# Optimization experiments

Hardware: AMD Instinct MI355X
Metric: run time of the kernel (lower is better)

The kernel has to match this reference:

```python
import math
import jax, jax.numpy as jnp
import numpy as np

DIM = 192
HEADS = 4
OUT_DIM = 192

def _conv(x, w, groups=1, pad=0):
    return jax.lax.conv_general_dilated(
        x, w, window_strides=(1, 1), padding=[(pad, pad), (pad, pad)],
        feature_group_count=groups, dimension_numbers=('NCHW', 'OIHW', 'NCHW'))

def setup_inputs() -> dict:
    key = jax.random.key(0)
    ks = jax.random.split(key, 8)
    b, c, h, w = 8, DIM, 128, 128
    x = jax.random.normal(ks[0], (b, c, h, w), dtype=jnp.float32)
    y = jax.random.normal(ks[1], (b, c, h, w), dtype=jnp.float32)
    s = 0.02
    kv_w = jax.random.normal(ks[2], (2 * DIM, DIM, 1, 1), dtype=jnp.float32) * s
    kv_dw_w = jax.random.normal(ks[3], (2 * DIM, 1, 3, 3), dtype=jnp.float32) * s  # depthwise, groups=2*dim
    q_w = jax.random.normal(ks[4], (DIM, DIM, 1, 1), dtype=jnp.float32) * s
    q_dw_w = jax.random.normal(ks[5], (DIM, DIM, 3, 3), dtype=jnp.float32) * s  # dense 3x3 (groups=1 in source)
    proj_w = jax.random.normal(ks[6], (OUT_DIM, DIM, 1, 1), dtype=jnp.float32) * s
    temperature = jnp.ones((HEADS, 1, 1), dtype=jnp.float32)
    return {"x": x, "y": y, "kv_w": kv_w, "kv_dw_w": kv_dw_w, "q_w": q_w,
            "q_dw_w": q_dw_w, "proj_w": proj_w, "temperature": temperature}

def _l2norm(t, eps=1e-12):
    # matches torch F.normalize(dim=-1)
    n = jnp.sqrt(jnp.sum(t * t, axis=-1, keepdims=True))
    return t / jnp.maximum(n, eps)

def reference(x, y, kv_w, kv_dw_w, q_w, q_dw_w, proj_w, temperature):
    b, c, h, w = x.shape
    hw = h * w
    ch = c // HEADS  # channels per head
    kv = _conv(_conv(x, kv_w), kv_dw_w, groups=2 * c, pad=1)  # [b, 2c, h, w]
    k, v = jnp.split(kv, 2, axis=1)
    q = _conv(_conv(y, q_w), q_dw_w, pad=1)  # [b, c, h, w]
    # b (head ch) h w -> b head ch (h w)
    q = q.reshape(b, HEADS, ch, hw)
    k = k.reshape(b, HEADS, ch, hw)
    v = v.reshape(b, HEADS, ch, hw)
    q = _l2norm(q)
    k = _l2norm(k)
    attn = jnp.einsum('bhcn,bhdn->bhcd', q, k)  # channel-wise attention [b,H,ch,ch]
    temp = temperature * math.log(attn.shape[-1])  # [H,1,1]
    attn = jax.nn.softmax(attn * temp[None], axis=-1)
    out = jnp.einsum('bhcd,bhdn->bhcn', attn, v)  # [b,H,ch,hw]
    out = out.reshape(b, c, h, w)
    return _conv(out, proj_w)
```

## Files before the change

### kernel.cpp

```cpp
#include <hip/hip_runtime.h>


#define HW 16384

using f32x4  = __attribute__((ext_vector_type(4))) float;
using bf16x8 = __attribute__((ext_vector_type(8))) __bf16;
using u16x8  = __attribute__((ext_vector_type(8))) unsigned short;
typedef unsigned short u16;

__device__ __forceinline__ u16 f2bf(float f) {
  unsigned u = __builtin_bit_cast(unsigned, f);
  u = (u + 0x7fffu + ((u >> 16) & 1u)) >> 16;
  return (u16)u;
}
__device__ __forceinline__ float bf2f(u16 s) {
  unsigned u = ((unsigned)s) << 16;
  return __builtin_bit_cast(float, u);
}

__device__ __forceinline__ void g2l16(const void* g, void* l) {
  __builtin_amdgcn_global_load_lds(
      (const __attribute__((address_space(1))) unsigned int*)g,
      (__attribute__((address_space(3))) unsigned int*)l, 16, 0, 0);
}

__global__ __launch_bounds__(256) void pack_w1(
    const float* __restrict__ kv_w, u16* __restrict__ W1) {
  int i = blockIdx.x * 256 + threadIdx.x;
  W1[i] = f2bf(kv_w[i]);
}

__global__ __launch_bounds__(192) void make_w4(
    const float* __restrict__ q_w, const float* __restrict__ q_dw_w,
    u16* __restrict__ W4) {
  const int o = blockIdx.x / 9, seg = blockIdx.x % 9;
  const int c = threadIdx.x;
  float s = 0.f;
  for (int ic = 0; ic < 192; ++ic)
    s += q_dw_w[(o * 192 + ic) * 9 + seg] * q_w[ic * 192 + c];
  W4[o * 1728 + seg * 192 + c] = f2bf(s);
}

template <typename TIn>
__global__ __launch_bounds__(256) void transpose_kernel(
    const TIn* __restrict__ src, u16* __restrict__ dst, int srcCstride) {
  __shared__ u16 tile[32][34];
  const int bz = blockIdx.z;
  const int n0 = blockIdx.x * 32;
  const int c0 = blockIdx.y * 32;
  const TIn* s = src + (long)bz * srcCstride * HW;
  u16* d = dst + (long)bz * HW * 192;
  const int tx = threadIdx.x & 31;
  const int ty = threadIdx.x >> 5;
#pragma unroll
  for (int i = 0; i < 32; i += 8) {
    if constexpr (sizeof(TIn) == 4)
      tile[ty + i][tx] = f2bf(((const float*)s)[(long)(c0 + ty + i) * HW + n0 + tx]);
    else
      tile[ty + i][tx] = ((const u16*)s)[(long)(c0 + ty + i) * HW + n0 + tx];
  }
  __syncthreads();
#pragma unroll
  for (int i = 0; i < 32; i += 8)
    d[(long)(n0 + ty + i) * 192 + c0 + tx] = tile[tx][ty + i];
}

template <int NSEG, bool OUT_BF16, bool FUSE_RQ>
__global__ __launch_bounds__(256, 2) void gemm_kernel(
    const u16* __restrict__ A, const u16* __restrict__ Bt,
    void* __restrict__ Cout, const u16* __restrict__ zp,
    int M, long aBatchStride, float* __restrict__ rqs) {
  __shared__ __align__(16) u16 shA[2][4096];
  __shared__ __align__(16) u16 shB[2][16384];
  const int Ktot = NSEG * 192;
  const int NT = NSEG * 3;
  const int tid = threadIdx.x;
  const int w = tid >> 6;
  const int lane = tid & 63;
  const int rl = lane & 15;
  const int q4 = lane >> 4;
  const int wm = w & 1, wn = w >> 1;
  const int b = blockIdx.z;
  const int n0 = blockIdx.x * 256;
  const int m0 = blockIdx.y * 64;

  const u16* Ab = A + (long)b * aBatchStride + (long)m0 * Ktot;
  const u16* Btb = Bt + (long)b * HW * 192;
  const char* asrc = (const char*)(Ab + (long)(w * 16 + rl) * Ktot) + q4 * 16;
  const char* zpp = (const char*)zp + q4 * 16;

  const char* p0[4];
  int xx[4], yy[4];
#pragma unroll
  for (int j = 0; j < 4; ++j) {
    int n = n0 + (w * 4 + j) * 16 + rl;
    p0[j] = (const char*)(Btb + (long)n * 192) + q4 * 16;
    xx[j] = n & 127;
    yy[j] = n >> 7;
  }

  f32x4 acc[2][8];
#pragma unroll
  for (int i = 0; i < 2; ++i)
#pragma unroll
    for (int j = 0; j < 8; ++j) acc[i][j] = f32x4{0.f, 0.f, 0.f, 0.f};

  const int lane_off = lane * 8;

  auto stage = [&](int t, int sbuf) {
    const long ao = (long)t * 128;
    g2l16(asrc + ao, &shA[sbuf][w * 1024]);
    g2l16(asrc + ao + 64, &shA[sbuf][w * 1024 + 512]);
    const char* bp[4];
    int kb;
    if constexpr (NSEG == 1) {
      kb = t * 128;
#pragma unroll
      for (int j = 0; j < 4; ++j) bp[j] = p0[j];
    } else {
      const int seg = t / 3;
      kb = (t - seg * 3) * 128;
      const int dy = seg / 3 - 1, dx = seg % 3 - 1;
      const int roff = (dy * 128 + dx) * 384;
#pragma unroll
      for (int j = 0; j < 4; ++j) {
        bool ok = ((unsigned)(xx[j] + dx) < 128u) && ((unsigned)(yy[j] + dy) < 128u);
        bp[j] = ok ? p0[j] + roff : zpp;
      }
    }
#pragma unroll
    for (int j = 0; j < 4; ++j) {
      g2l16(bp[j] + kb, &shB[sbuf][(w * 4 + j) * 1024]);
      g2l16(bp[j] + kb + 64, &shB[sbuf][(w * 4 + j) * 1024 + 512]);
    }
  };

  auto compute = [&](int cbuf) {
    bf16x8 af[2][2];
#pragma unroll
    for (int i = 0; i < 2; ++i)
#pragma unroll
      for (int h = 0; h < 2; ++h)
        af[i][h] = *(const bf16x8*)&shA[cbuf][(wm * 2 + i) * 1024 + h * 512 + lane_off];
#pragma unroll
    for (int jh = 0; jh < 2; ++jh) {
      bf16x8 bfr[4][2];
#pragma unroll
      for (int j2 = 0; j2 < 4; ++j2)
#pragma unroll
        for (int h = 0; h < 2; ++h)
          bfr[j2][h] = *(const bf16x8*)&shB[cbuf][(wn * 8 + jh * 4 + j2) * 1024 + h * 512 + lane_off];
#pragma unroll
      for (int i = 0; i < 2; ++i)
#pragma unroll
        for (int j2 = 0; j2 < 4; ++j2) {
          const int j = jh * 4 + j2;
          acc[i][j] = __builtin_amdgcn_mfma_f32_16x16x32_bf16(af[i][0], bfr[j2][0], acc[i][j], 0, 0, 0);
          acc[i][j] = __builtin_amdgcn_mfma_f32_16x16x32_bf16(af[i][1], bfr[j2][1], acc[i][j], 0, 0, 0);
        }
    }
  };

  stage(0, 0);
  __syncthreads();
  int cur = 0;
  for (int t = 0; t < NT - 1; ++t) {
    stage(t + 1, cur ^ 1);
    compute(cur);
    __syncthreads();
    cur ^= 1;
  }
  compute(cur);

  const int mb = m0 + wm * 32;
  const int nb = n0 + wn * 128;
  if constexpr (OUT_BF16) {
    u16* Cb = (u16*)Cout + (long)b * M * HW;
#pragma unroll
    for (int i = 0; i < 2; ++i)
#pragma unroll
      for (int j = 0; j < 8; ++j)
#pragma unroll
        for (int r = 0; r < 4; ++r)
          Cb[(long)(mb + i * 16 + q4 * 4 + r) * HW + nb + j * 16 + rl] = f2bf(acc[i][j][r]);
  } else {
    float* Cb = (float*)Cout + (long)b * M * HW;
#pragma unroll
    for (int i = 0; i < 2; ++i)
#pragma unroll
      for (int j = 0; j < 8; ++j)
#pragma unroll
        for (int r = 0; r < 4; ++r)
          Cb[(long)(mb + i * 16 + q4 * 4 + r) * HW + nb + j * 16 + rl] = acc[i][j][r];
  }
  if constexpr (FUSE_RQ) {
#pragma unroll
    for (int i = 0; i < 2; ++i)
#pragma unroll
      for (int r = 0; r < 4; ++r) {
        float s = 0.f;
#pragma unroll
        for (int j = 0; j < 8; ++j) s += acc[i][j][r] * acc[i][j][r];
        s += __shfl_xor(s, 1, 64);
        s += __shfl_xor(s, 2, 64);
        s += __shfl_xor(s, 4, 64);
        s += __shfl_xor(s, 8, 64);
        if (rl == 0)
          atomicAdd(&rqs[b * 192 + mb + i * 16 + q4 * 4 + r], s);
      }
  }
}

template <bool FUSE_NORM>
__global__ __launch_bounds__(256) void dwconv_kernel(
    const u16* __restrict__ kv, const float* __restrict__ dww,
    u16* __restrict__ dst, int cbase, int dstCstride, float* __restrict__ rks) {
  __shared__ __align__(16) u16 sp[HW];
  const int c = blockIdx.x;
  const int b = blockIdx.y;
  const int c2 = cbase + c;
  const u16* src = kv + ((long)b * 384 + c2) * HW;
  u16* out = dst + ((long)b * dstCstride + c) * HW;
  const int tid = threadIdx.x;
#pragma unroll
  for (int it = 0; it < 8; ++it)
    ((u16x8*)sp)[it * 256 + tid] = ((const u16x8*)src)[it * 256 + tid];
  __syncthreads();
  float w9[9];
#pragma unroll
  for (int t = 0; t < 9; ++t) w9[t] = dww[c2 * 9 + t];
  float ssum = 0.f;
  for (int o = 0; o < 8; ++o) {
    const int base = o * 2048 + tid * 8;
    const int yy = base >> 7;
    const int x0 = base & 127;
    float vv[3][10];
#pragma unroll
    for (int r = 0; r < 3; ++r) {
      int yr = yy + r - 1;
      if (yr >= 0 && yr < 128) {
        const u16* rp = sp + yr * 128 + x0;
        u16x8 mid = *(const u16x8*)rp;
#pragma unroll
        for (int i2 = 0; i2 < 8; ++i2) vv[r][1 + i2] = bf2f(mid[i2]);
        vv[r][0] = (x0 > 0)   ? bf2f(rp[-1]) : 0.f;
        vv[r][9] = (x0 < 120) ? bf2f(rp[8])  : 0.f;
      } else {
#pragma unroll
        for (int i2 = 0; i2 < 10; ++i2) vv[r][i2] = 0.f;
      }
    }
    u16x8 ov;
#pragma unroll
    for (int i2 = 0; i2 < 8; ++i2) {
      float s = 0.f;
#pragma unroll
      for (int r = 0; r < 3; ++r)
#pragma unroll
        for (int d = 0; d < 3; ++d) s += w9[r * 3 + d] * vv[r][i2 + d];
      if constexpr (FUSE_NORM) ssum += s * s;
      ov[i2] = f2bf(s);
    }
    *(u16x8*)(out + base) = ov;
  }
  if constexpr (FUSE_NORM) {
#pragma unroll
    for (int off = 32; off; off >>= 1) ssum += __shfl_down(ssum, off, 64);
    if ((tid & 63) == 0) atomicAdd(&rks[b * 192 + c], ssum);
  }
}

__global__ __launch_bounds__(256) void gram_kernel(
    const u16* __restrict__ qq, const u16* __restrict__ kk, float* __restrict__ gram) {
  __shared__ float red[4 * 2304];
  const int bh = blockIdx.x;
  const int kc = blockIdx.y;
  const int b = bh >> 2, h = bh & 3;
  const u16* qb = qq + ((long)b * 192 + h * 48) * HW;
  const u16* kb = kk + ((long)b * 192 + h * 48) * HW;
  const int tid = threadIdx.x, w = tid >> 6, lane = tid & 63;
  const int rl = lane & 15, q4 = lane >> 4;
  f32x4 acc[3][3];
#pragma unroll
  for (int i = 0; i < 3; ++i)
#pragma unroll
    for (int j = 0; j < 3; ++j) acc[i][j] = f32x4{0.f, 0.f, 0.f, 0.f};
  for (int tt = 0; tt < 16; ++tt) {
    const int k0 = ((kc * 16 + tt) * 4 + w) * 32 + q4 * 8;
    bf16x8 af[3], bfr[3];
#pragma unroll
    for (int i = 0; i < 3; ++i) af[i] = *(const bf16x8*)(qb + (long)(i * 16 + rl) * HW + k0);
#pragma unroll
    for (int j = 0; j < 3; ++j) bfr[j] = *(const bf16x8*)(kb + (long)(j * 16 + rl) * HW + k0);
#pragma unroll
    for (int i = 0; i < 3; ++i)
#pragma unroll
      for (int j = 0; j < 3; ++j)
        acc[i][j] = __builtin_amdgcn_mfma_f32_16x16x32_bf16(af[i], bfr[j], acc[i][j], 0, 0, 0);
  }
#pragma unroll
  for (int i = 0; i < 3; ++i)
#pragma unroll
    for (int j = 0; j < 3; ++j)
#pragma unroll
      for (int r = 0; r < 4; ++r)
        red[w * 2304 + (i * 16 + q4 * 4 + r) * 48 + j * 16 + rl] = acc[i][j][r];
  __syncthreads();
  for (int e = tid; e < 2304; e += 256)
    atomicAdd(&gram[(long)bh * 2304 + e], red[e] + red[2304 + e] + red[4608 + e] + red[6912 + e]);
}

__global__ __launch_bounds__(64) void softmax_kernel(
    const float* __restrict__ gram, const float* __restrict__ rqs,
    const float* __restrict__ rks, const float* __restrict__ temperature,
    float* __restrict__ attn) {
  const int R = blockIdx.x;
  const int lane = threadIdx.x;
  const int b = R / 192;
  const int h = (R % 192) / 48;
  const float ts = temperature[h] * 3.8712010109078907f;
  const float rq = rsqrtf(fmaxf(rqs[R], 1e-24f));
  float val = -3.0e38f;
  if (lane < 48) {
    const float rk = rsqrtf(fmaxf(rks[b * 192 + h * 48 + lane], 1e-24f));
    val = gram[(long)R * 48 + lane] * rq * rk * ts;
  }
  float mx = val;
#pragma unroll
  for (int off = 32; off; off >>= 1) mx = fmaxf(mx, __shfl_xor(mx, off, 64));
  float ex = (lane < 48) ? expf(val - mx) : 0.f;
  float sm = ex;
#pragma unroll
  for (int off = 32; off; off >>= 1) sm += __shfl_xor(sm, off, 64);
  if (lane < 48) attn[(long)R * 48 + lane] = ex / sm;
}

__global__ __launch_bounds__(192) void pa_kernel(
    const float* __restrict__ proj_w, const float* __restrict__ attn,
    u16* __restrict__ PA) {
  const int b = blockIdx.x;
  const int o = blockIdx.y;
  const int dg = threadIdx.x;
  const int hg = dg / 48, dl = dg % 48;
  const float* arow = attn + ((long)(b * 4 + hg) * 48) * 48 + dl;
  const float* prow = proj_w + o * 192 + hg * 48;
  float s = 0.f;
#pragma unroll
  for (int cl = 0; cl < 48; ++cl) s += prow[cl] * arow[(long)cl * 48];
  PA[((long)b * 192 + o) * 192 + dg] = f2bf(s);
}

extern "C" void kernel_launch(void* const* d_in, const int* in_sizes, int n_in,
                              void* d_out, int out_size, void* d_ws, size_t ws_size,
                              hipStream_t stream) {
  (void)in_sizes; (void)n_in; (void)out_size; (void)ws_size;
  const float* x        = (const float*)d_in[0];
  const float* y        = (const float*)d_in[1];
  const float* kv_w     = (const float*)d_in[2];
  const float* kv_dw_w  = (const float*)d_in[3];
  const float* q_w      = (const float*)d_in[4];
  const float* q_dw_w   = (const float*)d_in[5];
  const float* proj_w   = (const float*)d_in[6];
  const float* temperature = (const float*)d_in[7];

  char* ws = (char*)d_ws;
  u16* KV = (u16*)(ws + 0L);
  u16* R0 = (u16*)(ws + 100663296L);
  u16* R1 = (u16*)(ws + 150994944L);
  u16* R2 = (u16*)(ws + 201326592L);
  char* tail = ws + 251658240L;
  u16*   zp   = (u16*)(tail + 0);
  float* rqs  = (float*)(tail + 512);
  float* rks  = (float*)(tail + 6656);
  float* gram = (float*)(tail + 12800);
  float* attn = (float*)(tail + 307712);
  u16*   W1   = (u16*)(tail + 602624);
  u16*   W4   = (u16*)(tail + 750080);
  u16*   PA   = (u16*)(tail + 1413632);

  hipMemsetAsync(tail, 0, 307712, stream);
  pack_w1<<<288, 256, 0, stream>>>(kv_w, W1);
  make_w4<<<1728, 192, 0, stream>>>(q_w, q_dw_w, W4);

  transpose_kernel<float><<<dim3(512, 6, 8), 256, 0, stream>>>(y, R2, 192);
  gemm_kernel<9, true, true><<<dim3(64, 3, 8), 256, 0, stream>>>(W4, R2, R1, zp, 192, 0, rqs);

  transpose_kernel<float><<<dim3(512, 6, 8), 256, 0, stream>>>(x, R2, 192);
  gemm_kernel<1, true, false><<<dim3(64, 6, 8), 256, 0, stream>>>(W1, R2, KV, zp, 384, 0, nullptr);
  dwconv_kernel<true><<<dim3(192, 8), 256, 0, stream>>>(KV, kv_dw_w, R0, 0, 192, rks);
  dwconv_kernel<false><<<dim3(192, 8), 256, 0, stream>>>(KV, kv_dw_w, KV, 192, 384, nullptr);
  transpose_kernel<u16><<<dim3(512, 6, 8), 256, 0, stream>>>(KV, R2, 384);

  gram_kernel<<<dim3(32, 8), 256, 0, stream>>>(R1, R0, gram);
  softmax_kernel<<<1536, 64, 0, stream>>>(gram, rqs, rks, temperature, attn);
  pa_kernel<<<dim3(8, 192), 192, 0, stream>>>(proj_w, attn, PA);
  gemm_kernel<1, false, false><<<dim3(64, 3, 8), 256, 0, stream>>>(PA, R2, d_out, zp, 192, 36864, nullptr);
}
```

Baseline: 681.3 us.

## Enlarge GEMM tile to 192x256 with 512 threads and deeper async pipeline

```diff
diff --git a/kernel.cpp b/kernel.cpp
--- a/kernel.cpp
+++ b/kernel.cpp
@@ -66,11 +66,11 @@
 }
 
 template <int NSEG, bool OUT_BF16, bool FUSE_RQ>
-__global__ __launch_bounds__(256, 2) void gemm_kernel(
+__global__ __launch_bounds__(512, 2) void gemm_kernel(
     const u16* __restrict__ A, const u16* __restrict__ Bt,
     void* __restrict__ Cout, const u16* __restrict__ zp,
     int M, long aBatchStride, float* __restrict__ rqs) {
-  __shared__ __align__(16) u16 shA[2][4096];
+  __shared__ __align__(16) u16 shA[2][12288];
   __shared__ __align__(16) u16 shB[2][16384];
   const int Ktot = NSEG * 192;
   const int NT = NSEG * 3;
@@ -79,128 +79,135 @@
   const int lane = tid & 63;
   const int rl = lane & 15;
   const int q4 = lane >> 4;
-  const int wm = w & 1, wn = w >> 1;
+  const int wm = w >> 2, wn = w & 3;
   const int b = blockIdx.z;
   const int n0 = blockIdx.x * 256;
-  const int m0 = blockIdx.y * 64;
+  const int m0 = blockIdx.y * 192;
 
   const u16* Ab = A + (long)b * aBatchStride + (long)m0 * Ktot;
   const u16* Btb = Bt + (long)b * HW * 192;
-  const char* asrc = (const char*)(Ab + (long)(w * 16 + rl) * Ktot) + q4 * 16;
   const char* zpp = (const char*)zp + q4 * 16;
 
-  const char* p0[4];
-  int xx[4], yy[4];
-#pragma unroll
-  for (int j = 0; j < 4; ++j) {
-    int n = n0 + (w * 4 + j) * 16 + rl;
-    p0[j] = (const char*)(Btb + (long)n * 192) + q4 * 16;
-    xx[j] = n & 127;
-    yy[j] = n >> 7;
-  }
-
-  f32x4 acc[2][8];
-#pragma unroll
-  for (int i = 0; i < 2; ++i)
-#pragma unroll
-    for (int j = 0; j < 8; ++j) acc[i][j] = f32x4{0.f, 0.f, 0.f, 0.f};
+  const char* aptr0 = (const char*)(Ab + (long)(w * 16 + rl) * Ktot) + q4 * 16;
+  const char* aptr1 = (const char*)(Ab + (long)((8 + (w >> 1)) * 16 + rl) * Ktot)
+                      + q4 * 16 + (w & 1) * 64;
+
+  const char* p0b[2];
+  int xx[2], yy[2];
+#pragma unroll
+  for (int jj = 0; jj < 2; ++jj) {
+    int n = n0 + (2 * w + jj) * 16 + rl;
+    p0b[jj] = (const char*)(Btb + (long)n * 192) + q4 * 16;
+    xx[jj] = n & 127;
+    yy[jj] = n >> 7;
+  }
+
+  f32x4 acc[6][4];
+#pragma unroll
+  for (int i = 0; i < 6; ++i)
+#pragma unroll
+    for (int j = 0; j < 4; ++j) acc[i][j] = f32x4{0.f, 0.f, 0.f, 0.f};
 
   const int lane_off = lane * 8;
 
-  auto stage = [&](int t, int sbuf) {
-    const long ao = (long)t * 128;
-    g2l16(asrc + ao, &shA[sbuf][w * 1024]);
-    g2l16(asrc + ao + 64, &shA[sbuf][w * 1024 + 512]);
-    const char* bp[4];
-    int kb;
+  auto stage = [&](int tt, int sbuf) {
+    u16* dA = &shA[sbuf][0];
+    u16* dB = &shB[sbuf][0];
+    const long ao = (long)tt * 128;
+    g2l16(aptr0 + ao,      dA + (w * 2 + 0) * 512);
+    g2l16(aptr0 + ao + 64, dA + (w * 2 + 1) * 512);
+    g2l16(aptr1 + ao,      dA + ((8 + (w >> 1)) * 2 + (w & 1)) * 512);
     if constexpr (NSEG == 1) {
-      kb = t * 128;
-#pragma unroll
-      for (int j = 0; j < 4; ++j) bp[j] = p0[j];
+      const long kb = (long)tt * 128;
+#pragma unroll
+      for (int jj = 0; jj < 2; ++jj) {
+        g2l16(p0b[jj] + kb,      dB + ((2 * w + jj) * 2 + 0) * 512);
+        g2l16(p0b[jj] + kb + 64, dB + ((2 * w + jj) * 2 + 1) * 512);
+      }
     } else {
-      const int seg = t / 3;
-      kb = (t - seg * 3) * 128;
+      const int seg = tt / 3;
+      const long kb = (long)(tt - seg * 3) * 128;
       const int dy = seg / 3 - 1, dx = seg % 3 - 1;
-      const int roff = (dy * 128 + dx) * 384;
-#pragma unroll
-      for (int j = 0; j < 4; ++j) {
-        bool ok = ((unsigned)(xx[j] + dx) < 128u) && ((unsigned)(yy[j] + dy) < 128u);
-        bp[j] = ok ? p0[j] + roff : zpp;
+      const long roff = (long)(dy * 128 + dx) * 384;
+#pragma unroll
+      for (int jj = 0; jj < 2; ++jj) {
+        bool ok = ((unsigned)(xx[jj] + dx) < 128u) && ((unsigned)(yy[jj] + dy) < 128u);
+        const char* bp = ok ? p0b[jj] + roff : zpp;
+        g2l16(bp + kb,      dB + ((2 * w + jj) * 2 + 0) * 512);
+        g2l16(bp + kb + 64, dB + ((2 * w + jj) * 2 + 1) * 512);
       }
     }
-#pragma unroll
-    for (int j = 0; j < 4; ++j) {
-      g2l16(bp[j] + kb, &shB[sbuf][(w * 4 + j) * 1024]);
-      g2l16(bp[j] + kb + 64, &shB[sbuf][(w * 4 + j) * 1024 + 512]);
-    }
   };
 
   auto compute = [&](int cbuf) {
-    bf16x8 af[2][2];
-#pragma unroll
-    for (int i = 0; i < 2; ++i)
+    const u16* sA = &shA[cbuf][0];
+    const u16* sB = &shB[cbuf][0];
+    bf16x8 af[6][2];
+#pragma unroll
+    for (int i = 0; i < 6; ++i)
 #pragma unroll
       for (int h = 0; h < 2; ++h)
-        af[i][h] = *(const bf16x8*)&shA[cbuf][(wm * 2 + i) * 1024 + h * 512 + lane_off];
-#pragma unroll
-    for (int jh = 0; jh < 2; ++jh) {
-      bf16x8 bfr[4][2];
-#pragma unroll
-      for (int j2 = 0; j2 < 4; ++j2)
-#pragma unroll
-        for (int h = 0; h < 2; ++h)
-          bfr[j2][h] = *(const bf16x8*)&shB[cbuf][(wn * 8 + jh * 4 + j2) * 1024 + h * 512 + lane_off];
-#pragma unroll
-      for (int i = 0; i < 2; ++i)
-#pragma unroll
-        for (int j2 = 0; j2 < 4; ++j2) {
-          const int j = jh * 4 + j2;
-          acc[i][j] = __builtin_amdgcn_mfma_f32_16x16x32_bf16(af[i][0], bfr[j2][0], acc[i][j], 0, 0, 0);
-          acc[i][j] = __builtin_amdgcn_mfma_f32_16x16x32_bf16(af[i][1], bfr[j2][1], acc[i][j], 0, 0, 0);
-        }
-    }
+        af[i][h] = *(const bf16x8*)&sA[((wm * 6 + i) * 2 + h) * 512 + lane_off];
+    bf16x8 bfr[4][2];
+#pragma unroll
+    for (int j = 0; j < 4; ++j)
+#pragma unroll
+      for (int h = 0; h < 2; ++h)
+        bfr[j][h] = *(const bf16x8*)&sB[((wn * 4 + j) * 2 + h) * 512 + lane_off];
+#pragma unroll
+    for (int i = 0; i < 6; ++i)
+#pragma unroll
+      for (int j = 0; j < 4; ++j) {
+        acc[i][j] = __builtin_amdgcn_mfma_f32_16x16x32_bf16(af[i][0], bfr[j][0], acc[i][j], 0, 0, 0);
+        acc[i][j] = __builtin_amdgcn_mfma_f32_16x16x32_bf16(af[i][1], bfr[j][1], acc[i][j], 0, 0, 0);
+      }
   };
 
   stage(0, 0);
-  __syncthreads();
-  int cur = 0;
-  for (int t = 0; t < NT - 1; ++t) {
-    stage(t + 1, cur ^ 1);
+  stage(1, 1);
+  for (int t = 0; t < NT; ++t) {
+    const int cur = t & 1;
+    if (t < NT - 1)
+      asm volatile("s_waitcnt vmcnt(7)" ::: "memory");
+    else
+      asm volatile("s_waitcnt vmcnt(0)" ::: "memory");
+    __builtin_amdgcn_s_barrier();
     compute(cur);
-    __syncthreads();
-    cur ^= 1;
-  }
-  compute(cur);
-
-  const int mb = m0 + wm * 32;
-  const int nb = n0 + wn * 128;
+    asm volatile("s_waitcnt lgkmcnt(0)" ::: "memory");
+    __builtin_amdgcn_sched_barrier(0);
+    __builtin_amdgcn_s_barrier();
+    if (t + 2 < NT) stage(t + 2, cur);
+  }
+
+  const int mb = m0 + wm * 96;
+  const int nb = n0 + wn * 64;
   if constexpr (OUT_BF16) {
     u16* Cb = (u16*)Cout + (long)b * M * HW;
 #pragma unroll
-    for (int i = 0; i < 2; ++i)
-#pragma unroll
-      for (int j = 0; j < 8; ++j)
+    for (int i = 0; i < 6; ++i)
+#pragma unroll
+      for (int j = 0; j < 4; ++j)
 #pragma unroll
         for (int r = 0; r < 4; ++r)
           Cb[(long)(mb + i * 16 + q4 * 4 + r) * HW + nb + j * 16 + rl] = f2bf(acc[i][j][r]);
   } else {
     float* Cb = (float*)Cout + (long)b * M * HW;
 #pragma unroll
-    for (int i = 0; i < 2; ++i)
-#pragma unroll
-      for (int j = 0; j < 8; ++j)
+    for (int i = 0; i < 6; ++i)
+#pragma unroll
+      for (int j = 0; j < 4; ++j)
 #pragma unroll
         for (int r = 0; r < 4; ++r)
           Cb[(long)(mb + i * 16 + q4 * 4 + r) * HW + nb + j * 16 + rl] = acc[i][j][r];
   }
   if constexpr (FUSE_RQ) {
 #pragma unroll
-    for (int i = 0; i < 2; ++i)
+    for (int i = 0; i < 6; ++i)
 #pragma unroll
       for (int r = 0; r < 4; ++r) {
         float s = 0.f;
 #pragma unroll
-        for (int j = 0; j < 8; ++j) s += acc[i][j][r] * acc[i][j][r];
+        for (int j = 0; j < 4; ++j) s += acc[i][j][r] * acc[i][j][r];
         s += __shfl_xor(s, 1, 64);
         s += __shfl_xor(s, 2, 64);
         s += __shfl_xor(s, 4, 64);
@@ -383,10 +390,10 @@
   make_w4<<<1728, 192, 0, stream>>>(q_w, q_dw_w, W4);
 
   transpose_kernel<float><<<dim3(512, 6, 8), 256, 0, stream>>>(y, R2, 192);
-  gemm_kernel<9, true, true><<<dim3(64, 3, 8), 256, 0, stream>>>(W4, R2, R1, zp, 192, 0, rqs);
+  gemm_kernel<9, true, true><<<dim3(64, 1, 8), 512, 0, stream>>>(W4, R2, R1, zp, 192, 0, rqs);
 
   transpose_kernel<float><<<dim3(512, 6, 8), 256, 0, stream>>>(x, R2, 192);
-  gemm_kernel<1, true, false><<<dim3(64, 6, 8), 256, 0, stream>>>(W1, R2, KV, zp, 384, 0, nullptr);
+  gemm_kernel<1, true, false><<<dim3(64, 2, 8), 512, 0, stream>>>(W1, R2, KV, zp, 384, 0, nullptr);
   dwconv_kernel<true><<<dim3(192, 8), 256, 0, stream>>>(KV, kv_dw_w, R0, 0, 192, rks);
   dwconv_kernel<false><<<dim3(192, 8), 256, 0, stream>>>(KV, kv_dw_w, KV, 192, 384, nullptr);
   transpose_kernel<u16><<<dim3(512, 6, 8), 256, 0, stream>>>(KV, R2, 384);
@@ -394,5 +401,5 @@
   gram_kernel<<<dim3(32, 8), 256, 0, stream>>>(R1, R0, gram);
   softmax_kernel<<<1536, 64, 0, stream>>>(gram, rqs, rks, temperature, attn);
   pa_kernel<<<dim3(8, 192), 192, 0, stream>>>(proj_w, attn, PA);
-  gemm_kernel<1, false, false><<<dim3(64, 3, 8), 256, 0, stream>>>(PA, R2, d_out, zp, 192, 36864, nullptr);
-}
+  gemm_kernel<1, false, false><<<dim3(64, 1, 8), 512, 0, stream>>>(PA, R2, d_out, zp, 192, 36864, nullptr);
+}
```

Result: faster. 643.1 us (-5.6%).
